# Kernel tuning notes

Measured on AMD Instinct MI355X. Metric: run time of the kernel, lower is better.

Reference implementation:

```python
import jax, jax.numpy as jnp
import numpy as np

HIDDEN = 1024
HEADS = 16
HEAD_DIM = HIDDEN // HEADS
SCALE = HEAD_DIM ** (-0.5)


def setup_inputs() -> dict:
    key = jax.random.key(0)
    ks = jax.random.split(key, 5)
    B, N, C = 8, 1024, HIDDEN
    x = jax.random.normal(ks[0], (B, N, C), dtype=jnp.float32)
    # torch nn.Linear params: weight [out, in], bias [out]
    w_in = jax.random.normal(ks[1], (3 * C, C), dtype=jnp.float32) * (C ** -0.5)
    b_in = jax.random.normal(ks[2], (3 * C,), dtype=jnp.float32) * 0.02
    w_out = jax.random.normal(ks[3], (C, C), dtype=jnp.float32) * (C ** -0.5)
    b_out = jax.random.normal(ks[4], (C,), dtype=jnp.float32) * 0.02
    return {"x": x, "w_in": w_in, "b_in": b_in, "w_out": w_out, "b_out": b_out}


def reference(x, w_in, b_in, w_out, b_out):
    B, N, C = x.shape
    H, D = HEADS, HEAD_DIM
    # in_proj: [B,N,3C] -> (3,B,H,N,D)
    qkv = x @ w_in.T + b_in
    qkv = qkv.reshape(B, N, 3, H, D).transpose(2, 0, 3, 1, 4)
    q, k, v = qkv[0], qkv[1], qkv[2]
    # attention scores scaled after QK^T (same math as scaling q)
    attn = jnp.einsum("bhnd,bhmd->bhnm", q, k) * SCALE
    attn = jax.nn.softmax(attn, axis=-1)
    out = jnp.einsum("bhnm,bhmd->bhnd", attn, v)  # [B,H,N,D]
    out = out.transpose(0, 2, 1, 3).reshape(B, N, C)
    return out @ w_out.T + b_out
```

## Files before the change

kernel.cpp:

```cpp
#include <hip/hip_runtime.h>


typedef __attribute__((ext_vector_type(8))) __bf16 bf16x8;
typedef __attribute__((ext_vector_type(4))) __bf16 bf16x4;
typedef __attribute__((ext_vector_type(4))) float f32x4;
typedef __attribute__((ext_vector_type(4))) short short4v;

__device__ __forceinline__ f32x4 mfma16(bf16x8 a, bf16x8 b, f32x4 c) {
  return __builtin_amdgcn_mfma_f32_16x16x32_bf16(a, b, c, 0, 0, 0);
}

#if __has_builtin(__builtin_amdgcn_mfma_f32_16x16x16bf16_1k)
__device__ __forceinline__ f32x4 mfma_pv(bf16x4 a, bf16x4 b, f32x4 c) {
  short4v as = __builtin_bit_cast(short4v, a);
  short4v bs = __builtin_bit_cast(short4v, b);
  return __builtin_amdgcn_mfma_f32_16x16x16bf16_1k(as, bs, c, 0, 0, 0);
}
#else
__device__ __forceinline__ f32x4 mfma_pv(bf16x4 a, bf16x4 b, f32x4 c) {
  __bf16 z = (__bf16)0.f;
  bf16x8 a8 = {a[0], a[1], a[2], a[3], z, z, z, z};
  bf16x8 b8 = {b[0], b[1], b[2], b[3], z, z, z, z};
  return mfma16(a8, b8, c);
}
#endif

__device__ __forceinline__ float fexp2(float x) {
#if __has_builtin(__builtin_amdgcn_exp2f)
  return __builtin_amdgcn_exp2f(x);
#else
  return exp2f(x);
#endif
}

typedef __attribute__((address_space(1))) const unsigned int gu32;
typedef __attribute__((address_space(3))) unsigned int lu32;

__device__ __forceinline__ void async16(const void* g, void* l) {
  __builtin_amdgcn_global_load_lds((gu32*)g, (lu32*)l, 16, 0, 0);
}

__global__ __launch_bounds__(256) void cvt_all(const float* __restrict__ x,
                                               __bf16* __restrict__ xb,
                                               const float* __restrict__ wi,
                                               __bf16* __restrict__ wib,
                                               const float* __restrict__ wo,
                                               __bf16* __restrict__ wob) {
  int blk = blockIdx.x;
  const float* in;
  __bf16* out;
  int base;
  if (blk < 4096)      { in = x;  out = xb;  base = 0; }
  else if (blk < 5632) { in = wi; out = wib; base = 4096; }
  else                 { in = wo; out = wob; base = 5632; }
  int i = ((blk - base) * 256 + threadIdx.x) * 8;
  float4 a = *(const float4*)(in + i);
  float4 b = *(const float4*)(in + i + 4);
  bf16x8 o;
  o[0] = (__bf16)a.x; o[1] = (__bf16)a.y; o[2] = (__bf16)a.z; o[3] = (__bf16)a.w;
  o[4] = (__bf16)b.x; o[5] = (__bf16)b.y; o[6] = (__bf16)b.z; o[7] = (__bf16)b.w;
  *(bf16x8*)(out + i) = o;
}

template <int NB, bool WRITE_VT, typename OutT>
__global__ __launch_bounds__(256) void gemm_nt(const __bf16* __restrict__ A,
                                               const __bf16* __restrict__ Bm,
                                               const float* __restrict__ bias,
                                               OutT* __restrict__ C, int K, int ldc,
                                               __bf16* __restrict__ vt) {
  __shared__ __bf16 As[128 * 64];
  __shared__ __bf16 Bs[NB * 32 * 64];
  const int t = threadIdx.x;
  const int wv = t >> 6, lane = t & 63;
  const int q16 = lane & 15, quad = lane >> 4;
  const int wm = wv >> 1, wn = wv & 1;
  const long m0 = (long)blockIdx.x * 128;
  const long n0 = (long)blockIdx.y * (NB * 32);

  f32x4 zero = {0.f, 0.f, 0.f, 0.f};
  f32x4 acc[4][NB];
#pragma unroll
  for (int i = 0; i < 4; ++i)
#pragma unroll
    for (int j = 0; j < NB; ++j) acc[i][j] = zero;

  char* AsB = (char*)As;
  char* BsB = (char*)Bs;
  const int sr = t >> 3;
  const int gc = (t & 7) ^ (sr & 7);

  for (int kt = 0; kt < K; kt += 64) {
    __syncthreads();
#pragma unroll
    for (int i = 0; i < 4; ++i)
      async16(A + (m0 + i * 32 + sr) * K + kt + gc * 8, AsB + i * 4096 + wv * 1024);
#pragma unroll
    for (int i = 0; i < NB; ++i)
      async16(Bm + (n0 + i * 32 + sr) * K + kt + gc * 8, BsB + i * 4096 + wv * 1024);
    __syncthreads();

#pragma unroll
    for (int kk = 0; kk < 2; ++kk) {
      bf16x8 af[4], bf[NB];
#pragma unroll
      for (int i = 0; i < 4; ++i) {
        int ra = wm * 64 + i * 16 + q16;
        af[i] = *(const bf16x8*)(AsB + ra * 128 + (((kk * 4 + quad) ^ (ra & 7)) * 16));
      }
#pragma unroll
      for (int j = 0; j < NB; ++j) {
        int rb = wn * (NB * 16) + j * 16 + q16;
        bf[j] = *(const bf16x8*)(BsB + rb * 128 + (((kk * 4 + quad) ^ (rb & 7)) * 16));
      }
#pragma unroll
      for (int i = 0; i < 4; ++i)
#pragma unroll
        for (int j = 0; j < NB; ++j) acc[i][j] = mfma16(af[i], bf[j], acc[i][j]);
    }
  }

  if (WRITE_VT && n0 >= 2048) {
    const int b = (int)(m0 >> 10);
    const int nbase = (int)(m0 - (long)b * 1024) + wm * 64;
#pragma unroll
    for (int j = 0; j < NB; ++j) {
      int col = (int)n0 + wn * (NB * 16) + j * 16 + q16;
      int cc = col - 2048;
      int h = cc >> 6, d = cc & 63;
      float bs = bias[col];
      __bf16* vrow = vt + (((long)(b * 16 + h)) << 16) + (long)d * 1024;
#pragma unroll
      for (int i = 0; i < 4; ++i) {
        int n = nbase + i * 16 + quad * 4;
        bf16x4 o;
#pragma unroll
        for (int r = 0; r < 4; ++r) o[r] = (__bf16)(acc[i][j][r] + bs);
        *(bf16x4*)(vrow + n) = o;
      }
    }
  } else {
#pragma unroll
    for (int j = 0; j < NB; ++j) {
      long col = n0 + wn * (NB * 16) + j * 16 + q16;
      float bs = bias[col];
#pragma unroll
      for (int i = 0; i < 4; ++i) {
        long rowb = m0 + wm * 64 + i * 16 + quad * 4;
#pragma unroll
        for (int r = 0; r < 4; ++r) {
          float v = acc[i][j][r] + bs;
          C[(rowb + r) * (long)ldc + col] = (OutT)v;
        }
      }
    }
  }
}

__global__ __launch_bounds__(256) void attn_kernel(const __bf16* __restrict__ qkv,
                                                   const __bf16* __restrict__ vt,
                                                   __bf16* __restrict__ ao) {
  __shared__ __bf16 Ks[64 * 64];
  __shared__ __bf16 Vt[64 * 64];
  const int t = threadIdx.x;
  const int wv = t >> 6, lane = t & 63;
  const int q16 = lane & 15, quad = lane >> 4;
  const int bh = blockIdx.x;
  const int b = bh >> 4, h = bh & 15;
  const int q0 = blockIdx.y * 64;
  const long rowbase = (long)b * 1024;

  bf16x8 qf0, qf1;
  {
    long qrow = rowbase + q0 + wv * 16 + q16;
    const __bf16* qp = qkv + qrow * 3072 + h * 64 + quad * 8;
    qf0 = *(const bf16x8*)qp;
    qf1 = *(const bf16x8*)(qp + 32);
#pragma unroll
    for (int j = 0; j < 8; ++j) {
      qf0[j] = (__bf16)((float)qf0[j] * 0.18033688f);
      qf1[j] = (__bf16)((float)qf1[j] * 0.18033688f);
    }
  }

  f32x4 zero = {0.f, 0.f, 0.f, 0.f};
  f32x4 oacc[4];
#pragma unroll
  for (int dt = 0; dt < 4; ++dt) oacc[dt] = zero;
  float lcol = 0.f;

  char* KsB = (char*)Ks;
  char* VtB = (char*)Vt;
  const int sr = t >> 3;
  const int sgc = (t & 7) ^ (sr & 7);
  const int sw = q16 & 7;

  for (int kv0 = 0; kv0 < 1024; kv0 += 64) {
    __syncthreads();
    const __bf16* kg = qkv + (rowbase + kv0 + sr) * 3072 + 1024 + h * 64 + sgc * 8;
    async16(kg, KsB + wv * 1024);
    async16(kg + (long)32 * 3072, KsB + 4096 + wv * 1024);
    const __bf16* vg = vt + (long)bh * 65536 + (long)sr * 1024 + kv0 + sgc * 8;
    async16(vg, VtB + wv * 1024);
    async16(vg + (long)32 * 1024, VtB + 4096 + wv * 1024);
    __syncthreads();

    f32x4 sacc[4];
#pragma unroll
    for (int nt = 0; nt < 4; ++nt) sacc[nt] = zero;
#pragma unroll
    for (int nt = 0; nt < 4; ++nt) {
      int kvr = nt * 16 + q16;
      bf16x8 kf0 = *(const bf16x8*)(KsB + kvr * 128 + ((quad ^ sw) * 16));
      bf16x8 kf1 = *(const bf16x8*)(KsB + kvr * 128 + (((4 + quad) ^ sw) * 16));
      sacc[nt] = mfma16(kf0, qf0, sacc[nt]);
      sacc[nt] = mfma16(kf1, qf1, sacc[nt]);
    }

    bf16x4 pf[4];
#pragma unroll
    for (int nt = 0; nt < 4; ++nt)
#pragma unroll
      for (int r = 0; r < 4; ++r) {
        float p = fexp2(sacc[nt][r]);
        lcol += p;
        pf[nt][r] = (__bf16)p;
      }

#pragma unroll
    for (int nt = 0; nt < 4; ++nt) {
      int c = ((nt * 2 + (quad >> 1)) ^ sw) * 16 + (quad & 1) * 8;
#pragma unroll
      for (int dt = 0; dt < 4; ++dt) {
        bf16x4 vf = *(const bf16x4*)(VtB + (dt * 16 + q16) * 128 + c);
        oacc[dt] = mfma_pv(pf[nt], vf, oacc[dt]);
      }
    }
  }

  lcol += __shfl_xor(lcol, 16);
  lcol += __shfl_xor(lcol, 32);
  float inv = 1.0f / lcol;
#pragma unroll
  for (int r = 0; r < 4; ++r) {
    float ir = __shfl(inv, quad * 4 + r);
    long orow = rowbase + q0 + wv * 16 + quad * 4 + r;
#pragma unroll
    for (int dt = 0; dt < 4; ++dt)
      ao[orow * 1024 + h * 64 + dt * 16 + q16] = (__bf16)(oacc[dt][r] * ir);
  }
}

extern "C" void kernel_launch(void* const* d_in, const int* in_sizes, int n_in,
                              void* d_out, int out_size, void* d_ws, size_t ws_size,
                              hipStream_t stream) {
  const float* x     = (const float*)d_in[0];
  const float* w_in  = (const float*)d_in[1];
  const float* b_in  = (const float*)d_in[2];
  const float* w_out = (const float*)d_in[3];
  const float* b_out = (const float*)d_in[4];
  float* out = (float*)d_out;

  char* ws = (char*)d_ws;
  __bf16* xb   = (__bf16*)(ws);
  __bf16* wib  = (__bf16*)(ws + 16777216);
  __bf16* wob  = (__bf16*)(ws + 23068672);
  __bf16* qkvb = (__bf16*)(ws + 25165824);
  __bf16* aob  = (__bf16*)(ws + 75497472);
  __bf16* vtg  = (__bf16*)d_out;

  cvt_all<<<6144, 256, 0, stream>>>(x, xb, w_in, wib, w_out, wob);
  gemm_nt<4, true, __bf16><<<dim3(64, 24), 256, 0, stream>>>(
      xb, wib, b_in, qkvb, 1024, 3072, vtg);
  attn_kernel<<<dim3(128, 16), 256, 0, stream>>>(qkvb, vtg, aob);
  gemm_nt<4, false, float><<<dim3(64, 8), 256, 0, stream>>>(
      aob, wob, b_out, out, 1024, 1024, nullptr);
}
```

Baseline: 243.9 us.

## Double query rows per attention block and add smaller-tile out-projection GEMM

The attention kernel now processes 128 query rows per block (two 16-row tiles per wave), so each K/V tile loaded into shared memory is reused for twice as many queries, and the grid is halved. A new 64x128-tile GEMM replaces the larger-tile kernel for the output projection, launching 1024 blocks instead of 512 to fill more compute units. The trade-off is higher register pressure in attention and less reuse per block in the out-projection.

```diff
diff --git a/kernel.cpp b/kernel.cpp
--- a/kernel.cpp
+++ b/kernel.cpp
@@ -156,6 +156,78 @@
   }
 }
 
+template <typename OutT>
+__global__ __launch_bounds__(256) void gemm_nt64(const __bf16* __restrict__ A,
+                                                 const __bf16* __restrict__ Bm,
+                                                 const float* __restrict__ bias,
+                                                 OutT* __restrict__ C, int K, int ldc) {
+  __shared__ __bf16 As[64 * 64];
+  __shared__ __bf16 Bs[128 * 64];
+  const int t = threadIdx.x;
+  const int wv = t >> 6, lane = t & 63;
+  const int q16 = lane & 15, quad = lane >> 4;
+  const int wm = wv >> 1, wn = wv & 1;
+  const long m0 = (long)blockIdx.x * 64;
+  const long n0 = (long)blockIdx.y * 128;
+
+  f32x4 zero = {0.f, 0.f, 0.f, 0.f};
+  f32x4 acc[2][4];
+#pragma unroll
+  for (int i = 0; i < 2; ++i)
+#pragma unroll
+    for (int j = 0; j < 4; ++j) acc[i][j] = zero;
+
+  char* AsB = (char*)As;
+  char* BsB = (char*)Bs;
+  const int sr = t >> 3;
+  const int gc = (t & 7) ^ (sr & 7);
+
+  for (int kt = 0; kt < K; kt += 64) {
+    __syncthreads();
+#pragma unroll
+    for (int i = 0; i < 2; ++i)
+      async16(A + (m0 + i * 32 + sr) * K + kt + gc * 8, AsB + i * 4096 + wv * 1024);
+#pragma unroll
+    for (int i = 0; i < 4; ++i)
+      async16(Bm + (n0 + i * 32 + sr) * K + kt + gc * 8, BsB + i * 4096 + wv * 1024);
+    __syncthreads();
+
+#pragma unroll
+    for (int kk = 0; kk < 2; ++kk) {
+      bf16x8 af[2], bf[4];
+#pragma unroll
+      for (int i = 0; i < 2; ++i) {
+        int ra = wm * 32 + i * 16 + q16;
+        af[i] = *(const bf16x8*)(AsB + ra * 128 + (((kk * 4 + quad) ^ (ra & 7)) * 16));
+      }
+#pragma unroll
+      for (int j = 0; j < 4; ++j) {
+        int rb = wn * 64 + j * 16 + q16;
+        bf[j] = *(const bf16x8*)(BsB + rb * 128 + (((kk * 4 + quad) ^ (rb & 7)) * 16));
+      }
+#pragma unroll
+      for (int i = 0; i < 2; ++i)
+#pragma unroll
+        for (int j = 0; j < 4; ++j) acc[i][j] = mfma16(af[i], bf[j], acc[i][j]);
+    }
+  }
+
+#pragma unroll
+  for (int j = 0; j < 4; ++j) {
+    long col = n0 + wn * 64 + j * 16 + q16;
+    float bs = bias[col];
+#pragma unroll
+    for (int i = 0; i < 2; ++i) {
+      long rowb = m0 + wm * 32 + i * 16 + quad * 4;
+#pragma unroll
+      for (int r = 0; r < 4; ++r) {
+        float v = acc[i][j][r] + bs;
+        C[(rowb + r) * (long)ldc + col] = (OutT)v;
+      }
+    }
+  }
+}
+
 __global__ __launch_bounds__(256) void attn_kernel(const __bf16* __restrict__ qkv,
                                                    const __bf16* __restrict__ vt,
                                                    __bf16* __restrict__ ao) {
@@ -166,27 +238,30 @@
   const int q16 = lane & 15, quad = lane >> 4;
   const int bh = blockIdx.x;
   const int b = bh >> 4, h = bh & 15;
-  const int q0 = blockIdx.y * 64;
+  const int q0 = blockIdx.y * 128;
   const long rowbase = (long)b * 1024;
 
-  bf16x8 qf0, qf1;
-  {
-    long qrow = rowbase + q0 + wv * 16 + q16;
+  bf16x8 qf[2][2];
+#pragma unroll
+  for (int qt = 0; qt < 2; ++qt) {
+    long qrow = rowbase + q0 + wv * 32 + qt * 16 + q16;
     const __bf16* qp = qkv + qrow * 3072 + h * 64 + quad * 8;
-    qf0 = *(const bf16x8*)qp;
-    qf1 = *(const bf16x8*)(qp + 32);
+    qf[qt][0] = *(const bf16x8*)qp;
+    qf[qt][1] = *(const bf16x8*)(qp + 32);
 #pragma unroll
     for (int j = 0; j < 8; ++j) {
-      qf0[j] = (__bf16)((float)qf0[j] * 0.18033688f);
-      qf1[j] = (__bf16)((float)qf1[j] * 0.18033688f);
+      qf[qt][0][j] = (__bf16)((float)qf[qt][0][j] * 0.18033688f);
+      qf[qt][1][j] = (__bf16)((float)qf[qt][1][j] * 0.18033688f);
     }
   }
 
   f32x4 zero = {0.f, 0.f, 0.f, 0.f};
-  f32x4 oacc[4];
-#pragma unroll
-  for (int dt = 0; dt < 4; ++dt) oacc[dt] = zero;
-  float lcol = 0.f;
+  f32x4 oacc[2][4];
+#pragma unroll
+  for (int qt = 0; qt < 2; ++qt)
+#pragma unroll
+    for (int dt = 0; dt < 4; ++dt) oacc[qt][dt] = zero;
+  float lcol[2] = {0.f, 0.f};
 
   char* KsB = (char*)Ks;
   char* VtB = (char*)Vt;
@@ -204,27 +279,34 @@
     async16(vg + (long)32 * 1024, VtB + 4096 + wv * 1024);
     __syncthreads();
 
-    f32x4 sacc[4];
-#pragma unroll
-    for (int nt = 0; nt < 4; ++nt) sacc[nt] = zero;
+    f32x4 sacc[2][4];
+#pragma unroll
+    for (int qt = 0; qt < 2; ++qt)
+#pragma unroll
+      for (int nt = 0; nt < 4; ++nt) sacc[qt][nt] = zero;
 #pragma unroll
     for (int nt = 0; nt < 4; ++nt) {
       int kvr = nt * 16 + q16;
       bf16x8 kf0 = *(const bf16x8*)(KsB + kvr * 128 + ((quad ^ sw) * 16));
       bf16x8 kf1 = *(const bf16x8*)(KsB + kvr * 128 + (((4 + quad) ^ sw) * 16));
-      sacc[nt] = mfma16(kf0, qf0, sacc[nt]);
-      sacc[nt] = mfma16(kf1, qf1, sacc[nt]);
-    }
-
-    bf16x4 pf[4];
-#pragma unroll
-    for (int nt = 0; nt < 4; ++nt)
-#pragma unroll
-      for (int r = 0; r < 4; ++r) {
-        float p = fexp2(sacc[nt][r]);
-        lcol += p;
-        pf[nt][r] = (__bf16)p;
-      }
+#pragma unroll
+      for (int qt = 0; qt < 2; ++qt) {
+        sacc[qt][nt] = mfma16(kf0, qf[qt][0], sacc[qt][nt]);
+        sacc[qt][nt] = mfma16(kf1, qf[qt][1], sacc[qt][nt]);
+      }
+    }
+
+    bf16x4 pf[2][4];
+#pragma unroll
+    for (int qt = 0; qt < 2; ++qt)
+#pragma unroll
+      for (int nt = 0; nt < 4; ++nt)
+#pragma unroll
+        for (int r = 0; r < 4; ++r) {
+          float p = fexp2(sacc[qt][nt][r]);
+          lcol[qt] += p;
+          pf[qt][nt][r] = (__bf16)p;
+        }
 
 #pragma unroll
     for (int nt = 0; nt < 4; ++nt) {
@@ -232,21 +314,27 @@
 #pragma unroll
       for (int dt = 0; dt < 4; ++dt) {
         bf16x4 vf = *(const bf16x4*)(VtB + (dt * 16 + q16) * 128 + c);
-        oacc[dt] = mfma_pv(pf[nt], vf, oacc[dt]);
-      }
-    }
-  }
-
-  lcol += __shfl_xor(lcol, 16);
-  lcol += __shfl_xor(lcol, 32);
-  float inv = 1.0f / lcol;
-#pragma unroll
-  for (int r = 0; r < 4; ++r) {
-    float ir = __shfl(inv, quad * 4 + r);
-    long orow = rowbase + q0 + wv * 16 + quad * 4 + r;
-#pragma unroll
-    for (int dt = 0; dt < 4; ++dt)
-      ao[orow * 1024 + h * 64 + dt * 16 + q16] = (__bf16)(oacc[dt][r] * ir);
+#pragma unroll
+        for (int qt = 0; qt < 2; ++qt)
+          oacc[qt][dt] = mfma_pv(pf[qt][nt], vf, oacc[qt][dt]);
+      }
+    }
+  }
+
+#pragma unroll
+  for (int qt = 0; qt < 2; ++qt) {
+    float l = lcol[qt];
+    l += __shfl_xor(l, 16);
+    l += __shfl_xor(l, 32);
+    float inv = 1.0f / l;
+#pragma unroll
+    for (int r = 0; r < 4; ++r) {
+      float ir = __shfl(inv, quad * 4 + r);
+      long orow = rowbase + q0 + wv * 32 + qt * 16 + quad * 4 + r;
+#pragma unroll
+      for (int dt = 0; dt < 4; ++dt)
+        ao[orow * 1024 + h * 64 + dt * 16 + q16] = (__bf16)(oacc[qt][dt][r] * ir);
+    }
   }
 }
 
@@ -271,7 +359,7 @@
   cvt_all<<<6144, 256, 0, stream>>>(x, xb, w_in, wib, w_out, wob);
   gemm_nt<4, true, __bf16><<<dim3(64, 24), 256, 0, stream>>>(
       xb, wib, b_in, qkvb, 1024, 3072, vtg);
-  attn_kernel<<<dim3(128, 16), 256, 0, stream>>>(qkvb, vtg, aob);
-  gemm_nt<4, false, float><<<dim3(64, 8), 256, 0, stream>>>(
-      aob, wob, b_out, out, 1024, 1024, nullptr);
-}
+  attn_kernel<<<dim3(128, 8), 256, 0, stream>>>(qkvb, vtg, aob);
+  gemm_nt64<float><<<dim3(128, 8), 256, 0, stream>>>(
+      aob, wob, b_out, out, 1024, 1024);
+}
```

Result: slower. 253.6 us (+4.0%).
